# Kernel optimization log

Hardware: AMD Instinct MI355X
Metric: run time of the kernel (lower is better)

Reference implementation:

```python
import jax, jax.numpy as jnp
import numpy as np

B, S, D, H, L = 16, 1024, 128, 8, 3
DFF = 4 * D  # 512
DH = D // H  # 16
NUM_CLASSES = 6


def layernorm(x, g, b, eps):
    mu = jnp.mean(x, axis=-1, keepdims=True)
    var = jnp.mean(jnp.square(x - mu), axis=-1, keepdims=True)
    return g * (x - mu) / jnp.sqrt(var + eps) + b


def setup_inputs() -> dict:
    key = jax.random.key(0)
    ks = jax.random.split(key, 16)
    sc = 0.05
    inp = {
        'x': jax.random.normal(ks[0], (B, S, D), dtype=jnp.float32),
        'Wq': jax.random.normal(ks[1], (L, D, D), dtype=jnp.float32) * sc,
        'bq': jnp.zeros((L, D), dtype=jnp.float32),
        'Wk': jax.random.normal(ks[2], (L, D, D), dtype=jnp.float32) * sc,
        'bk': jnp.zeros((L, D), dtype=jnp.float32),
        'Wv': jax.random.normal(ks[3], (L, D, D), dtype=jnp.float32) * sc,
        'bv': jnp.zeros((L, D), dtype=jnp.float32),
        'ln1_g': jnp.ones((L, D), dtype=jnp.float32),
        'ln1_b': jnp.zeros((L, D), dtype=jnp.float32),
        'W1': jax.random.normal(ks[4], (L, D, DFF), dtype=jnp.float32) * sc,
        'b1': jnp.zeros((L, DFF), dtype=jnp.float32),
        'W2': jax.random.normal(ks[5], (L, DFF, D), dtype=jnp.float32) * sc,
        'b2': jnp.zeros((L, D), dtype=jnp.float32),
        'ln2_g': jnp.ones((L, D), dtype=jnp.float32),
        'ln2_b': jnp.zeros((L, D), dtype=jnp.float32),
        'Wout': jax.random.normal(ks[6], (D, NUM_CLASSES), dtype=jnp.float32) * sc,
        'bout': jnp.zeros((NUM_CLASSES,), dtype=jnp.float32),
    }
    return inp


def reference(x, Wq, bq, Wk, bk, Wv, bv, ln1_g, ln1_b, W1, b1, W2, b2, ln2_g, ln2_b, Wout, bout):
    scale = 1.0 / jnp.sqrt(jnp.float32(DH))
    for l in range(L):
        # Q/K/V projections with ReLU activation (as in source Dense(..., relu))
        q = jax.nn.relu(jnp.einsum('bsd,de->bse', x, Wq[l]) + bq[l])
        k = jax.nn.relu(jnp.einsum('bsd,de->bse', x, Wk[l]) + bk[l])
        v = jax.nn.relu(jnp.einsum('bsd,de->bse', x, Wv[l]) + bv[l])
        # split-heads (tf.split axis=-1 / concat axis=0 == reshape to heads)
        qh = q.reshape(B, S, H, DH)
        kh = k.reshape(B, S, H, DH)
        vh = v.reshape(B, S, H, DH)
        scores = jnp.einsum('bqhd,bkhd->bhqk', qh, kh) * scale  # [B,H,S,S]
        attn = jax.nn.softmax(scores, axis=-1)
        o = jnp.einsum('bhqk,bkhd->bqhd', attn, vh).reshape(B, S, D)
        x = layernorm(o + x, ln1_g[l], ln1_b[l], 1e-8)
        # pointwise FFN (Conv1D kernel_size=1 == dense over last dim)
        h = jax.nn.relu(jnp.einsum('bsd,df->bsf', x, W1[l]) + b1[l])
        f = jnp.einsum('bsf,fd->bsd', h, W2[l]) + b2[l]
        x = layernorm(f + x, ln2_g[l], ln2_b[l], 1e-6)
    return jnp.einsum('bsd,dc->bsc', x, Wout) + bout
```

## Files before the change

kernel.cpp:

```cpp
#include <hip/hip_runtime.h>
#include <math.h>

#define Bq 16
#define Sq 1024
#define Dq 128
#define Hq 8
#define DHq 16
#define DFFq 512
#define Lq 3
#define NCLS 6
#define NROWS (Bq * Sq)
#define NX ((size_t)NROWS * Dq)

typedef __attribute__((ext_vector_type(8))) short    bf16x8;
typedef __attribute__((ext_vector_type(4))) float    f32x4;
typedef __attribute__((ext_vector_type(4))) _Float16 f16x4;
typedef __attribute__((ext_vector_type(8))) _Float16 f16x8;

__device__ inline ushort f32_to_bf16(float f) {
    union { float f; unsigned u; } v; v.f = f;
    unsigned r = v.u + 0x7fffu + ((v.u >> 16) & 1u);
    return (ushort)(r >> 16);
}

__global__ __launch_bounds__(256) void prep_kernel(
    const float* __restrict__ Wqp, const float* __restrict__ Wkp,
    const float* __restrict__ Wvp, const float* __restrict__ W1p,
    const float* __restrict__ W2p, const float* __restrict__ xp,
    ushort* __restrict__ wbf, ushort* __restrict__ xbf)
{
    const int gid = blockIdx.x * 256 + threadIdx.x;
    if (gid < 147456) {
        const int w   = gid / 49152;
        const int rem = gid - w * 49152;
        const int l   = rem >> 14;
        const int idx = rem & 16383;
        const int k   = idx >> 7;
        const int n   = idx & 127;
        const float* src = (w == 0) ? Wqp : (w == 1) ? Wkp : Wvp;
        const float scl = (w == 0) ? 0.25f : 1.0f;
        wbf[(size_t)(w * 3 + l) * 16384 + n * 128 + k] =
            f32_to_bf16(src[(size_t)l * 16384 + k * 128 + n] * scl);
    } else if (gid < 344064) {
        const int g   = gid - 147456;
        const int l   = g >> 16;
        const int idx = g & 65535;
        const int k   = idx >> 9;
        const int n   = idx & 511;
        wbf[147456 + (size_t)l * 65536 + n * 128 + k] =
            f32_to_bf16(W1p[(size_t)l * 65536 + k * 512 + n]);
    } else if (gid < 540672) {
        const int g   = gid - 344064;
        const int l   = g >> 16;
        const int idx = g & 65535;
        const int k   = idx >> 7;
        const int n   = idx & 127;
        wbf[344064 + (size_t)l * 65536 + n * 512 + k] =
            f32_to_bf16(W2p[(size_t)l * 65536 + k * 128 + n]);
    } else {
        const int g = gid - 540672;
        xbf[g] = f32_to_bf16(xp[g]);
    }
}

__global__ __launch_bounds__(256) void gemm_qkv(
    const ushort* __restrict__ A,
    const ushort* __restrict__ wq, const ushort* __restrict__ wk,
    const ushort* __restrict__ wv,
    const float* __restrict__ bqp, const float* __restrict__ bkp,
    const float* __restrict__ bvp,
    _Float16* __restrict__ qo, _Float16* __restrict__ ko,
    _Float16* __restrict__ vo)
{
    __shared__ ushort As[64 * 40];
    __shared__ ushort Bs[128 * 40];

    const int sel  = blockIdx.y;
    const ushort* Bt   = (sel == 0) ? wq : (sel == 1) ? wk : wv;
    const float*  bias = (sel == 0) ? bqp : (sel == 1) ? bkp : bvp;
    const float   bscl = (sel == 0) ? 0.25f : 1.0f;

    const int tid  = threadIdx.x;
    const int row0 = blockIdx.x * 64;
    const int wave = tid >> 6;
    const int lane = tid & 63;
    const int quad = lane >> 4;
    const int m16  = lane & 15;
    const int wm   = wave >> 1;
    const int wn   = wave & 1;

    const int sar = tid >> 2;
    const int sac = (tid & 3) * 8;

    f32x4 acc[2][4];
    #pragma unroll
    for (int i = 0; i < 2; ++i)
        #pragma unroll
        for (int j = 0; j < 4; ++j) acc[i][j] = (f32x4)0.f;

    for (int k0 = 0; k0 < 128; k0 += 32) {
        bf16x8 av = *(const bf16x8*)(A + (size_t)(row0 + sar) * 128 + k0 + sac);
        const int r1 = tid >> 2, r2 = r1 + 64;
        bf16x8 bv1 = *(const bf16x8*)(Bt + (size_t)r1 * 128 + k0 + sac);
        bf16x8 bv2 = *(const bf16x8*)(Bt + (size_t)r2 * 128 + k0 + sac);

        __syncthreads();
        *(bf16x8*)&As[sar * 40 + sac] = av;
        *(bf16x8*)&Bs[r1 * 40 + sac]  = bv1;
        *(bf16x8*)&Bs[r2 * 40 + sac]  = bv2;
        __syncthreads();

        bf16x8 af[2], bf[4];
        #pragma unroll
        for (int i = 0; i < 2; ++i)
            af[i] = *(const bf16x8*)&As[(32 * wm + 16 * i + m16) * 40 + quad * 8];
        #pragma unroll
        for (int j = 0; j < 4; ++j)
            bf[j] = *(const bf16x8*)&Bs[(64 * wn + 16 * j + m16) * 40 + quad * 8];
        #pragma unroll
        for (int i = 0; i < 2; ++i)
            #pragma unroll
            for (int j = 0; j < 4; ++j)
                acc[i][j] = __builtin_amdgcn_mfma_f32_16x16x32_bf16(af[i], bf[j], acc[i][j], 0, 0, 0);
    }

    #pragma unroll
    for (int i = 0; i < 2; ++i) {
        #pragma unroll
        for (int j = 0; j < 4; ++j) {
            const int col = 64 * wn + 16 * j + m16;
            const float bb = bias[col] * bscl;
            const int hh = col >> 4, dh = col & 15;
            #pragma unroll
            for (int r = 0; r < 4; ++r) {
                float val = fmaxf(acc[i][j][r] + bb, 0.f);
                const int gr = row0 + 32 * wm + 16 * i + quad * 4 + r;
                const int b = gr >> 10, s = gr & 1023;
                if (sel == 2) {
                    vo[(((size_t)b * Hq + hh) * DHq + dh) * Sq + s] = (_Float16)val;
                } else {
                    _Float16* outp = (sel == 0) ? qo : ko;
                    outp[(((size_t)b * Hq + hh) * Sq + s) * DHq + dh] = (_Float16)val;
                }
            }
        }
    }
}

__global__ __launch_bounds__(256) void gemm_ffn_fused(
    const float* __restrict__ o, const float* __restrict__ resid,
    const float* __restrict__ g1, const float* __restrict__ beta1,
    const ushort* __restrict__ W1t, const float* __restrict__ bias1,
    const ushort* __restrict__ W2t, const float* __restrict__ bias2,
    const float* __restrict__ g2, const float* __restrict__ beta2,
    float* __restrict__ xb, ushort* __restrict__ xbbf,
    const float* __restrict__ Wout, const float* __restrict__ bout,
    float* __restrict__ out, int last)
{
    __shared__ __align__(16) char smem[69120];
    ushort*    Af   = (ushort*)smem;
    ushort*    Hs   = (ushort*)(smem + 8704);
    ushort*    Bs   = (ushort*)(smem + 41984);
    float*     wo_s = (float*)(smem + 41984);
    _Float16*  vals = (_Float16*)(smem + 60416);
    float*     mus  = (float*)(smem + 68864);
    float*     rsds = (float*)(smem + 68992);

    const int tid  = threadIdx.x;
    const int row0 = blockIdx.x * 32;
    const int wave = tid >> 6;
    const int lane = tid & 63;
    const int quad = lane >> 4;
    const int m16  = lane & 15;
    const int wm   = wave >> 1;
    const int wn   = wave & 1;
    const int sac  = (tid & 3) * 8;
    const int r1   = tid >> 2, r2 = r1 + 64;

    #pragma unroll 2
    for (int it = 0; it < 8; ++it) {
        const int rr = wave * 8 + it;
        const size_t base = (size_t)(row0 + rr) * Dq;
        float v0 = o[base + lane]      + resid[base + lane];
        float v1 = o[base + 64 + lane] + resid[base + 64 + lane];

        float s = v0 + v1;
        #pragma unroll
        for (int off = 32; off > 0; off >>= 1) s += __shfl_xor(s, off, 64);
        const float mu = s * (1.f / 128.f);
        const float d0 = v0 - mu, d1 = v1 - mu;
        float vs = d0 * d0 + d1 * d1;
        #pragma unroll
        for (int off = 32; off > 0; off >>= 1) vs += __shfl_xor(vs, off, 64);
        const float rstd = rsqrtf(vs * (1.f / 128.f) + 1e-8f);

        const float rv0 = g1[lane]      * d0 * rstd + beta1[lane];
        const float rv1 = g1[lane + 64] * d1 * rstd + beta1[lane + 64];
        Af[rr * 136 + lane]       = f32_to_bf16(rv0);
        Af[rr * 136 + 64 + lane]  = f32_to_bf16(rv1);
        vals[rr * 132 + lane]     = (_Float16)rv0;
        vals[rr * 132 + 64 + lane]= (_Float16)rv1;
    }

    f32x4 acc[4];
    #pragma unroll
    for (int j = 0; j < 4; ++j) acc[j] = (f32x4)0.f;

    for (int idx = 0; idx < 8; ++idx) {
        const int cc = idx >> 1;
        const int k0 = (idx & 1) * 64;

        bf16x8 w11 = *(const bf16x8*)(W1t + (size_t)(cc * 128 + r1) * 128 + k0 + sac);
        bf16x8 w12 = *(const bf16x8*)(W1t + (size_t)(cc * 128 + r1) * 128 + k0 + 32 + sac);
        bf16x8 w21 = *(const bf16x8*)(W1t + (size_t)(cc * 128 + r2) * 128 + k0 + sac);
        bf16x8 w22 = *(const bf16x8*)(W1t + (size_t)(cc * 128 + r2) * 128 + k0 + 32 + sac);

        __syncthreads();
        *(bf16x8*)&Bs[r1 * 72 + sac]      = w11;
        *(bf16x8*)&Bs[r1 * 72 + 32 + sac] = w12;
        *(bf16x8*)&Bs[r2 * 72 + sac]      = w21;
        *(bf16x8*)&Bs[r2 * 72 + 32 + sac] = w22;
        __syncthreads();

        #pragma unroll
        for (int h = 0; h < 2; ++h) {
            const int kk = k0 + h * 32;
            const bf16x8 af = *(const bf16x8*)&Af[(16 * wm + m16) * 136 + kk + quad * 8];
            bf16x8 bf[4];
            #pragma unroll
            for (int j = 0; j < 4; ++j)
                bf[j] = *(const bf16x8*)&Bs[(64 * wn + 16 * j + m16) * 72 + h * 32 + quad * 8];
            #pragma unroll
            for (int j = 0; j < 4; ++j)
                acc[j] = __builtin_amdgcn_mfma_f32_16x16x32_bf16(af, bf[j], acc[j], 0, 0, 0);
        }

        if (idx & 1) {
            #pragma unroll
            for (int j = 0; j < 4; ++j) {
                const int col = cc * 128 + 64 * wn + 16 * j + m16;
                const float bb = bias1[col];
                #pragma unroll
                for (int r = 0; r < 4; ++r) {
                    const int row = 16 * wm + quad * 4 + r;
                    Hs[row * 520 + col] = f32_to_bf16(fmaxf(acc[j][r] + bb, 0.f));
                }
                acc[j] = (f32x4)0.f;
            }
        }
    }

    f32x4 acc2[4];
    #pragma unroll
    for (int j = 0; j < 4; ++j) acc2[j] = (f32x4)0.f;

    for (int kc = 0; kc < 8; ++kc) {
        const int k0 = kc * 64;

        bf16x8 w11 = *(const bf16x8*)(W2t + (size_t)r1 * DFFq + k0 + sac);
        bf16x8 w12 = *(const bf16x8*)(W2t + (size_t)r1 * DFFq + k0 + 32 + sac);
        bf16x8 w21 = *(const bf16x8*)(W2t + (size_t)r2 * DFFq + k0 + sac);
        bf16x8 w22 = *(const bf16x8*)(W2t + (size_t)r2 * DFFq + k0 + 32 + sac);

        __syncthreads();
        *(bf16x8*)&Bs[r1 * 72 + sac]      = w11;
        *(bf16x8*)&Bs[r1 * 72 + 32 + sac] = w12;
        *(bf16x8*)&Bs[r2 * 72 + sac]      = w21;
        *(bf16x8*)&Bs[r2 * 72 + 32 + sac] = w22;
        __syncthreads();

        #pragma unroll
        for (int h = 0; h < 2; ++h) {
            const int kk = k0 + h * 32;
            const bf16x8 af = *(const bf16x8*)&Hs[(16 * wm + m16) * 520 + kk + quad * 8];
            bf16x8 bf[4];
            #pragma unroll
            for (int j = 0; j < 4; ++j)
                bf[j] = *(const bf16x8*)&Bs[(64 * wn + 16 * j + m16) * 72 + h * 32 + quad * 8];
            #pragma unroll
            for (int j = 0; j < 4; ++j)
                acc2[j] = __builtin_amdgcn_mfma_f32_16x16x32_bf16(af, bf[j], acc2[j], 0, 0, 0);
        }
    }

    __syncthreads();

    float vreg[4][4];
    #pragma unroll
    for (int j = 0; j < 4; ++j) {
        const int col = 64 * wn + 16 * j + m16;
        const float bb = bias2[col];
        #pragma unroll
        for (int r = 0; r < 4; ++r) {
            const int row = 16 * wm + quad * 4 + r;
            float v = acc2[j][r] + bb + (float)vals[row * 132 + col];
            vreg[j][r] = v;
            vals[row * 132 + col] = (_Float16)v;
        }
    }
    if (last) {
        #pragma unroll
        for (int i = 0; i < 3; ++i) wo_s[tid + i * 256] = Wout[tid + i * 256];
    }
    __syncthreads();

    if (tid < 32) {
        float s = 0.f, s2 = 0.f;
        #pragma unroll 8
        for (int c = 0; c < Dq; ++c) {
            float x = (float)vals[tid * 132 + c];
            s += x; s2 = fmaf(x, x, s2);
        }
        const float mu  = s * (1.f / 128.f);
        const float var = s2 * (1.f / 128.f) - mu * mu;
        mus[tid]  = mu;
        rsds[tid] = rsqrtf(var + 1e-6f);
    }
    __syncthreads();

    if (!last) {
        #pragma unroll
        for (int j = 0; j < 4; ++j) {
            const int col = 64 * wn + 16 * j + m16;
            #pragma unroll
            for (int r = 0; r < 4; ++r) {
                const int row = 16 * wm + quad * 4 + r;
                const float rn = g2[col] * (vreg[j][r] - mus[row]) * rsds[row] + beta2[col];
                const size_t idx = (size_t)(row0 + row) * Dq + col;
                xb[idx]   = rn;
                xbbf[idx] = f32_to_bf16(rn);
            }
        }
    } else {
        #pragma unroll
        for (int j = 0; j < 4; ++j) {
            const int col = 64 * wn + 16 * j + m16;
            #pragma unroll
            for (int r = 0; r < 4; ++r) {
                const int row = 16 * wm + quad * 4 + r;
                vals[row * 132 + col] =
                    (_Float16)(g2[col] * (vreg[j][r] - mus[row]) * rsds[row] + beta2[col]);
            }
        }
        __syncthreads();
        if (tid < 32 * NCLS) {
            const int row = tid / NCLS;
            const int c   = tid - row * NCLS;
            float a = bout[c];
            #pragma unroll 8
            for (int kk = 0; kk < Dq; ++kk)
                a = fmaf((float)vals[row * 132 + kk], wo_s[kk * NCLS + c], a);
            out[(size_t)(row0 + row) * NCLS + c] = a;
        }
    }
}

__global__ __launch_bounds__(256) void attn_mfma(
    const _Float16* __restrict__ q, const _Float16* __restrict__ k,
    const _Float16* __restrict__ vt, float* __restrict__ o)
{
    __shared__ _Float16 Ks[256 * 20];
    __shared__ _Float16 Vs[16 * 264];

    const int bh   = blockIdx.x;
    const int qc   = blockIdx.y;
    const int b    = bh >> 3;
    const int h    = bh & 7;
    const int tid  = threadIdx.x;
    const int wave = tid >> 6;
    const int lane = tid & 63;
    const int quad = lane >> 4;
    const int m16  = lane & 15;
    const int q0   = qc * 128 + wave * 32;

    const f16x4 qf0 = *(const f16x4*)(q + (((size_t)bh * Sq) + q0 + m16) * DHq + quad * 4);
    const f16x4 qf1 = *(const f16x4*)(q + (((size_t)bh * Sq) + q0 + 16 + m16) * DHq + quad * 4);

    const _Float16* kg  = k  + (size_t)bh * Sq * DHq;
    const _Float16* vtg = vt + (size_t)bh * DHq * Sq;

    f32x4 oacc0 = (f32x4)0.f, oacc1 = (f32x4)0.f;
    float lacc0 = 0.f, lacc1 = 0.f;

    const int krow = tid;
    const int vrow = tid >> 4;
    const int vcol = (tid & 15) * 16;

    for (int kb = 0; kb < 4; ++kb) {
        f16x8 ka  = *(const f16x8*)(kg + ((size_t)kb * 256 + krow) * DHq);
        f16x8 kb8 = *(const f16x8*)(kg + ((size_t)kb * 256 + krow) * DHq + 8);
        f16x8 va  = *(const f16x8*)(vtg + (size_t)vrow * Sq + kb * 256 + vcol);
        f16x8 vb  = *(const f16x8*)(vtg + (size_t)vrow * Sq + kb * 256 + vcol + 8);
        __syncthreads();
        *(f16x8*)&Ks[krow * 20 + 0] = ka;
        *(f16x8*)&Ks[krow * 20 + 8] = kb8;
        *(f16x8*)&Vs[vrow * 264 + vcol + 0] = va;
        *(f16x8*)&Vs[vrow * 264 + vcol + 8] = vb;
        __syncthreads();

        #pragma unroll 4
        for (int kt = 0; kt < 16; ++kt) {
            const f16x4 kf = *(const f16x4*)&Ks[(kt * 16 + m16) * 20 + quad * 4];
            const f16x4 vf = *(const f16x4*)&Vs[m16 * 264 + kt * 16 + quad * 4];

            f32x4 st0 = __builtin_amdgcn_mfma_f32_16x16x16f16(kf, qf0, (f32x4)0.f, 0, 0, 0);
            f32x4 st1 = __builtin_amdgcn_mfma_f32_16x16x16f16(kf, qf1, (f32x4)0.f, 0, 0, 0);

            float p00 = __expf(st0[0]);
            float p01 = __expf(st0[1]);
            float p02 = __expf(st0[2]);
            float p03 = __expf(st0[3]);
            float p10 = __expf(st1[0]);
            float p11 = __expf(st1[1]);
            float p12 = __expf(st1[2]);
            float p13 = __expf(st1[3]);
            lacc0 += (p00 + p01) + (p02 + p03);
            lacc1 += (p10 + p11) + (p12 + p13);

            f16x4 pf0, pf1;
            pf0[0] = (_Float16)p00; pf0[1] = (_Float16)p01;
            pf0[2] = (_Float16)p02; pf0[3] = (_Float16)p03;
            pf1[0] = (_Float16)p10; pf1[1] = (_Float16)p11;
            pf1[2] = (_Float16)p12; pf1[3] = (_Float16)p13;

            oacc0 = __builtin_amdgcn_mfma_f32_16x16x16f16(pf0, vf, oacc0, 0, 0, 0);
            oacc1 = __builtin_amdgcn_mfma_f32_16x16x16f16(pf1, vf, oacc1, 0, 0, 0);
        }
    }

    lacc0 += __shfl_xor(lacc0, 16, 64);
    lacc0 += __shfl_xor(lacc0, 32, 64);
    lacc1 += __shfl_xor(lacc1, 16, 64);
    lacc1 += __shfl_xor(lacc1, 32, 64);

    #pragma unroll
    for (int r = 0; r < 4; ++r) {
        const float ls0 = __shfl(lacc0, quad * 4 + r, 64);
        const float ls1 = __shfl(lacc1, quad * 4 + r, 64);
        o[((size_t)b * Sq + q0 + quad * 4 + r) * Dq + h * DHq + m16]      = oacc0[r] / ls0;
        o[((size_t)b * Sq + q0 + 16 + quad * 4 + r) * Dq + h * DHq + m16] = oacc1[r] / ls1;
    }
}

extern "C" void kernel_launch(void* const* d_in, const int* in_sizes, int n_in,
                              void* d_out, int out_size, void* d_ws, size_t ws_size,
                              hipStream_t stream)
{
    const float* x_in  = (const float*)d_in[0];
    const float* Wq    = (const float*)d_in[1];
    const float* bq    = (const float*)d_in[2];
    const float* Wk    = (const float*)d_in[3];
    const float* bk    = (const float*)d_in[4];
    const float* Wv    = (const float*)d_in[5];
    const float* bv    = (const float*)d_in[6];
    const float* ln1_g = (const float*)d_in[7];
    const float* ln1_b = (const float*)d_in[8];
    const float* W1    = (const float*)d_in[9];
    const float* b1    = (const float*)d_in[10];
    const float* W2    = (const float*)d_in[11];
    const float* b2    = (const float*)d_in[12];
    const float* ln2_g = (const float*)d_in[13];
    const float* ln2_b = (const float*)d_in[14];
    const float* Wout  = (const float*)d_in[15];
    const float* bout  = (const float*)d_in[16];
    float* out = (float*)d_out;

    float* ws = (float*)d_ws;
    _Float16* qf16 = (_Float16*)ws;
    _Float16* kf16 = (_Float16*)(ws + NX / 2);
    _Float16* vt16 = (_Float16*)(ws + NX);
    float*    xb   = ws + 9 * NX / 2;
    ushort*   xbf0 = (ushort*)(ws + 11 * NX / 2);
    ushort*   xbbf = (ushort*)(ws + 13 * NX / 2);
    ushort*   wbf  = (ushort*)(ws + 7 * NX);
    float*    obuf = ws + 8 * NX;

    prep_kernel<<<dim3(10304), dim3(256), 0, stream>>>(Wq, Wk, Wv, W1, W2, x_in, wbf, xbf0);

    const dim3 blk(256);
    const float* xcur = x_in;
    const ushort* xcur_bf = xbf0;

    for (int l = 0; l < Lq; ++l) {
        const ushort* wqt = wbf + (size_t)(0 * 3 + l) * 16384;
        const ushort* wkt = wbf + (size_t)(1 * 3 + l) * 16384;
        const ushort* wvt = wbf + (size_t)(2 * 3 + l) * 16384;
        const ushort* w1t = wbf + 147456 + (size_t)l * 65536;
        const ushort* w2t = wbf + 344064 + (size_t)l * 65536;

        gemm_qkv<<<dim3(256, 3), blk, 0, stream>>>(
            xcur_bf, wqt, wkt, wvt, bq + l * Dq, bk + l * Dq, bv + l * Dq,
            qf16, kf16, vt16);

        attn_mfma<<<dim3(Bq * Hq, 8), blk, 0, stream>>>(qf16, kf16, vt16, obuf);

        gemm_ffn_fused<<<dim3(512), blk, 0, stream>>>(
            obuf, xcur, ln1_g + l * Dq, ln1_b + l * Dq,
            w1t, b1 + l * DFFq, w2t, b2 + l * Dq,
            ln2_g + l * Dq, ln2_b + l * Dq,
            xb, xbbf, Wout, bout, out, (l == Lq - 1) ? 1 : 0);

        xcur = xb;
        xcur_bf = xbbf;
    }
}
```

Measured before the change: 275.9 us.

## Fuse all layers into one persistent cooperative kernel with grid syncs

Replaces the ten separate launches (prep, then qkv/attention/ffn per layer) with a single cooperative persistent kernel of 512 blocks that loops over the work units of each stage and uses grid-wide barriers between stages. This targets per-launch overhead and the gaps between kernels. In exchange, every block is sized for the largest shared-memory stage, stages with uneven unit counts (768 qkv tiles, 1024 attention units) leave some blocks idle, and grid syncs have their own cost. If the cooperative launch fails, the code falls back to the old multi-kernel path.

```diff
diff --git a/kernel.cpp b/kernel.cpp
--- a/kernel.cpp
+++ b/kernel.cpp
@@ -1,5 +1,8 @@
 #include <hip/hip_runtime.h>
+#include <hip/hip_cooperative_groups.h>
 #include <math.h>
+
+namespace cg = cooperative_groups;
 
 #define Bq 16
 #define Sq 1024
@@ -11,6 +14,7 @@
 #define NCLS 6
 #define NROWS (Bq * Sq)
 #define NX ((size_t)NROWS * Dq)
+#define PREP_N 2637824
 
 typedef __attribute__((ext_vector_type(8))) short    bf16x8;
 typedef __attribute__((ext_vector_type(4))) float    f32x4;
@@ -23,13 +27,13 @@
     return (ushort)(r >> 16);
 }
 
-__global__ __launch_bounds__(256) void prep_kernel(
+__device__ __forceinline__ void prep_one(
+    int gid,
     const float* __restrict__ Wqp, const float* __restrict__ Wkp,
     const float* __restrict__ Wvp, const float* __restrict__ W1p,
     const float* __restrict__ W2p, const float* __restrict__ xp,
     ushort* __restrict__ wbf, ushort* __restrict__ xbf)
 {
-    const int gid = blockIdx.x * 256 + threadIdx.x;
     if (gid < 147456) {
         const int w   = gid / 49152;
         const int rem = gid - w * 49152;
@@ -63,7 +67,8 @@
     }
 }
 
-__global__ __launch_bounds__(256) void gemm_qkv(
+__device__ __forceinline__ void qkv_tile(
+    char* smem, int sel, int row0,
     const ushort* __restrict__ A,
     const ushort* __restrict__ wq, const ushort* __restrict__ wk,
     const ushort* __restrict__ wv,
@@ -72,25 +77,23 @@
     _Float16* __restrict__ qo, _Float16* __restrict__ ko,
     _Float16* __restrict__ vo)
 {
-    __shared__ ushort As[64 * 40];
-    __shared__ ushort Bs[128 * 40];
-
-    const int sel  = blockIdx.y;
+    ushort* As = (ushort*)smem;
+    ushort* Bs = (ushort*)smem + 2560;
+
     const ushort* Bt   = (sel == 0) ? wq : (sel == 1) ? wk : wv;
     const float*  bias = (sel == 0) ? bqp : (sel == 1) ? bkp : bvp;
     const float   bscl = (sel == 0) ? 0.25f : 1.0f;
 
     const int tid  = threadIdx.x;
-    const int row0 = blockIdx.x * 64;
     const int wave = tid >> 6;
     const int lane = tid & 63;
     const int quad = lane >> 4;
     const int m16  = lane & 15;
     const int wm   = wave >> 1;
     const int wn   = wave & 1;
-
-    const int sar = tid >> 2;
-    const int sac = (tid & 3) * 8;
+    const int sar  = tid >> 2;
+    const int sac  = (tid & 3) * 8;
+    const int r1   = tid >> 2, r2 = r1 + 64;
 
     f32x4 acc[2][4];
     #pragma unroll
@@ -99,8 +102,7 @@
         for (int j = 0; j < 4; ++j) acc[i][j] = (f32x4)0.f;
 
     for (int k0 = 0; k0 < 128; k0 += 32) {
-        bf16x8 av = *(const bf16x8*)(A + (size_t)(row0 + sar) * 128 + k0 + sac);
-        const int r1 = tid >> 2, r2 = r1 + 64;
+        bf16x8 av  = *(const bf16x8*)(A + (size_t)(row0 + sar) * 128 + k0 + sac);
         bf16x8 bv1 = *(const bf16x8*)(Bt + (size_t)r1 * 128 + k0 + sac);
         bf16x8 bv2 = *(const bf16x8*)(Bt + (size_t)r2 * 128 + k0 + sac);
 
@@ -147,7 +149,94 @@
     }
 }
 
-__global__ __launch_bounds__(256) void gemm_ffn_fused(
+__device__ __forceinline__ void attn_unit(
+    char* smem, int bh, int qc,
+    const _Float16* __restrict__ q, const _Float16* __restrict__ k,
+    const _Float16* __restrict__ vt, float* __restrict__ o)
+{
+    _Float16* Ks = (_Float16*)smem;
+    _Float16* Vs = (_Float16*)(smem + 10240);
+
+    const int b    = bh >> 3;
+    const int h    = bh & 7;
+    const int tid  = threadIdx.x;
+    const int wave = tid >> 6;
+    const int lane = tid & 63;
+    const int quad = lane >> 4;
+    const int m16  = lane & 15;
+    const int q0   = qc * 128 + wave * 32;
+
+    const f16x4 qf0 = *(const f16x4*)(q + (((size_t)bh * Sq) + q0 + m16) * DHq + quad * 4);
+    const f16x4 qf1 = *(const f16x4*)(q + (((size_t)bh * Sq) + q0 + 16 + m16) * DHq + quad * 4);
+
+    const _Float16* kg  = k  + (size_t)bh * Sq * DHq;
+    const _Float16* vtg = vt + (size_t)bh * DHq * Sq;
+
+    f32x4 oacc0 = (f32x4)0.f, oacc1 = (f32x4)0.f;
+    float lacc0 = 0.f, lacc1 = 0.f;
+
+    const int krow = tid;
+    const int vrow = tid >> 4;
+    const int vcol = (tid & 15) * 16;
+
+    for (int kb = 0; kb < 4; ++kb) {
+        f16x8 ka  = *(const f16x8*)(kg + ((size_t)kb * 256 + krow) * DHq);
+        f16x8 kb8 = *(const f16x8*)(kg + ((size_t)kb * 256 + krow) * DHq + 8);
+        f16x8 va  = *(const f16x8*)(vtg + (size_t)vrow * Sq + kb * 256 + vcol);
+        f16x8 vb  = *(const f16x8*)(vtg + (size_t)vrow * Sq + kb * 256 + vcol + 8);
+        __syncthreads();
+        *(f16x8*)&Ks[krow * 20 + 0] = ka;
+        *(f16x8*)&Ks[krow * 20 + 8] = kb8;
+        *(f16x8*)&Vs[vrow * 264 + vcol + 0] = va;
+        *(f16x8*)&Vs[vrow * 264 + vcol + 8] = vb;
+        __syncthreads();
+
+        #pragma unroll 4
+        for (int kt = 0; kt < 16; ++kt) {
+            const f16x4 kf = *(const f16x4*)&Ks[(kt * 16 + m16) * 20 + quad * 4];
+            const f16x4 vf = *(const f16x4*)&Vs[m16 * 264 + kt * 16 + quad * 4];
+
+            f32x4 st0 = __builtin_amdgcn_mfma_f32_16x16x16f16(kf, qf0, (f32x4)0.f, 0, 0, 0);
+            f32x4 st1 = __builtin_amdgcn_mfma_f32_16x16x16f16(kf, qf1, (f32x4)0.f, 0, 0, 0);
+
+            float p00 = __expf(st0[0]);
+            float p01 = __expf(st0[1]);
+            float p02 = __expf(st0[2]);
+            float p03 = __expf(st0[3]);
+            float p10 = __expf(st1[0]);
+            float p11 = __expf(st1[1]);
+            float p12 = __expf(st1[2]);
+            float p13 = __expf(st1[3]);
+            lacc0 += (p00 + p01) + (p02 + p03);
+            lacc1 += (p10 + p11) + (p12 + p13);
+
+            f16x4 pf0, pf1;
+            pf0[0] = (_Float16)p00; pf0[1] = (_Float16)p01;
+            pf0[2] = (_Float16)p02; pf0[3] = (_Float16)p03;
+            pf1[0] = (_Float16)p10; pf1[1] = (_Float16)p11;
+            pf1[2] = (_Float16)p12; pf1[3] = (_Float16)p13;
+
+            oacc0 = __builtin_amdgcn_mfma_f32_16x16x16f16(pf0, vf, oacc0, 0, 0, 0);
+            oacc1 = __builtin_amdgcn_mfma_f32_16x16x16f16(pf1, vf, oacc1, 0, 0, 0);
+        }
+    }
+
+    lacc0 += __shfl_xor(lacc0, 16, 64);
+    lacc0 += __shfl_xor(lacc0, 32, 64);
+    lacc1 += __shfl_xor(lacc1, 16, 64);
+    lacc1 += __shfl_xor(lacc1, 32, 64);
+
+    #pragma unroll
+    for (int r = 0; r < 4; ++r) {
+        const float ls0 = __shfl(lacc0, quad * 4 + r, 64);
+        const float ls1 = __shfl(lacc1, quad * 4 + r, 64);
+        o[((size_t)b * Sq + q0 + quad * 4 + r) * Dq + h * DHq + m16]      = oacc0[r] / ls0;
+        o[((size_t)b * Sq + q0 + 16 + quad * 4 + r) * Dq + h * DHq + m16] = oacc1[r] / ls1;
+    }
+}
+
+__device__ __forceinline__ void ffn_unit(
+    char* smem, int row0,
     const float* __restrict__ o, const float* __restrict__ resid,
     const float* __restrict__ g1, const float* __restrict__ beta1,
     const ushort* __restrict__ W1t, const float* __restrict__ bias1,
@@ -157,7 +246,6 @@
     const float* __restrict__ Wout, const float* __restrict__ bout,
     float* __restrict__ out, int last)
 {
-    __shared__ __align__(16) char smem[69120];
     ushort*    Af   = (ushort*)smem;
     ushort*    Hs   = (ushort*)(smem + 8704);
     ushort*    Bs   = (ushort*)(smem + 41984);
@@ -167,7 +255,6 @@
     float*     rsds = (float*)(smem + 68992);
 
     const int tid  = threadIdx.x;
-    const int row0 = blockIdx.x * 32;
     const int wave = tid >> 6;
     const int lane = tid & 63;
     const int quad = lane >> 4;
@@ -196,10 +283,10 @@
 
         const float rv0 = g1[lane]      * d0 * rstd + beta1[lane];
         const float rv1 = g1[lane + 64] * d1 * rstd + beta1[lane + 64];
-        Af[rr * 136 + lane]       = f32_to_bf16(rv0);
-        Af[rr * 136 + 64 + lane]  = f32_to_bf16(rv1);
-        vals[rr * 132 + lane]     = (_Float16)rv0;
-        vals[rr * 132 + 64 + lane]= (_Float16)rv1;
+        Af[rr * 136 + lane]        = f32_to_bf16(rv0);
+        Af[rr * 136 + 64 + lane]   = f32_to_bf16(rv1);
+        vals[rr * 132 + lane]      = (_Float16)rv0;
+        vals[rr * 132 + 64 + lane] = (_Float16)rv1;
     }
 
     f32x4 acc[4];
@@ -223,13 +310,13 @@
         __syncthreads();
 
         #pragma unroll
-        for (int h = 0; h < 2; ++h) {
-            const int kk = k0 + h * 32;
+        for (int hh = 0; hh < 2; ++hh) {
+            const int kk = k0 + hh * 32;
             const bf16x8 af = *(const bf16x8*)&Af[(16 * wm + m16) * 136 + kk + quad * 8];
             bf16x8 bf[4];
             #pragma unroll
             for (int j = 0; j < 4; ++j)
-                bf[j] = *(const bf16x8*)&Bs[(64 * wn + 16 * j + m16) * 72 + h * 32 + quad * 8];
+                bf[j] = *(const bf16x8*)&Bs[(64 * wn + 16 * j + m16) * 72 + hh * 32 + quad * 8];
             #pragma unroll
             for (int j = 0; j < 4; ++j)
                 acc[j] = __builtin_amdgcn_mfma_f32_16x16x32_bf16(af, bf[j], acc[j], 0, 0, 0);
@@ -270,13 +357,13 @@
         __syncthreads();
 
         #pragma unroll
-        for (int h = 0; h < 2; ++h) {
-            const int kk = k0 + h * 32;
+        for (int hh = 0; hh < 2; ++hh) {
+            const int kk = k0 + hh * 32;
             const bf16x8 af = *(const bf16x8*)&Hs[(16 * wm + m16) * 520 + kk + quad * 8];
             bf16x8 bf[4];
             #pragma unroll
             for (int j = 0; j < 4; ++j)
-                bf[j] = *(const bf16x8*)&Bs[(64 * wn + 16 * j + m16) * 72 + h * 32 + quad * 8];
+                bf[j] = *(const bf16x8*)&Bs[(64 * wn + 16 * j + m16) * 72 + hh * 32 + quad * 8];
             #pragma unroll
             for (int j = 0; j < 4; ++j)
                 acc2[j] = __builtin_amdgcn_mfma_f32_16x16x32_bf16(af, bf[j], acc2[j], 0, 0, 0);
@@ -355,91 +442,91 @@
     }
 }
 
-__global__ __launch_bounds__(256) void attn_mfma(
-    const _Float16* __restrict__ q, const _Float16* __restrict__ k,
-    const _Float16* __restrict__ vt, float* __restrict__ o)
-{
-    __shared__ _Float16 Ks[256 * 20];
-    __shared__ _Float16 Vs[16 * 264];
-
-    const int bh   = blockIdx.x;
-    const int qc   = blockIdx.y;
-    const int b    = bh >> 3;
-    const int h    = bh & 7;
-    const int tid  = threadIdx.x;
-    const int wave = tid >> 6;
-    const int lane = tid & 63;
-    const int quad = lane >> 4;
-    const int m16  = lane & 15;
-    const int q0   = qc * 128 + wave * 32;
-
-    const f16x4 qf0 = *(const f16x4*)(q + (((size_t)bh * Sq) + q0 + m16) * DHq + quad * 4);
-    const f16x4 qf1 = *(const f16x4*)(q + (((size_t)bh * Sq) + q0 + 16 + m16) * DHq + quad * 4);
-
-    const _Float16* kg  = k  + (size_t)bh * Sq * DHq;
-    const _Float16* vtg = vt + (size_t)bh * DHq * Sq;
-
-    f32x4 oacc0 = (f32x4)0.f, oacc1 = (f32x4)0.f;
-    float lacc0 = 0.f, lacc1 = 0.f;
-
-    const int krow = tid;
-    const int vrow = tid >> 4;
-    const int vcol = (tid & 15) * 16;
-
-    for (int kb = 0; kb < 4; ++kb) {
-        f16x8 ka  = *(const f16x8*)(kg + ((size_t)kb * 256 + krow) * DHq);
-        f16x8 kb8 = *(const f16x8*)(kg + ((size_t)kb * 256 + krow) * DHq + 8);
-        f16x8 va  = *(const f16x8*)(vtg + (size_t)vrow * Sq + kb * 256 + vcol);
-        f16x8 vb  = *(const f16x8*)(vtg + (size_t)vrow * Sq + kb * 256 + vcol + 8);
-        __syncthreads();
-        *(f16x8*)&Ks[krow * 20 + 0] = ka;
-        *(f16x8*)&Ks[krow * 20 + 8] = kb8;
-        *(f16x8*)&Vs[vrow * 264 + vcol + 0] = va;
-        *(f16x8*)&Vs[vrow * 264 + vcol + 8] = vb;
-        __syncthreads();
-
-        #pragma unroll 4
-        for (int kt = 0; kt < 16; ++kt) {
-            const f16x4 kf = *(const f16x4*)&Ks[(kt * 16 + m16) * 20 + quad * 4];
-            const f16x4 vf = *(const f16x4*)&Vs[m16 * 264 + kt * 16 + quad * 4];
-
-            f32x4 st0 = __builtin_amdgcn_mfma_f32_16x16x16f16(kf, qf0, (f32x4)0.f, 0, 0, 0);
-            f32x4 st1 = __builtin_amdgcn_mfma_f32_16x16x16f16(kf, qf1, (f32x4)0.f, 0, 0, 0);
-
-            float p00 = __expf(st0[0]);
-            float p01 = __expf(st0[1]);
-            float p02 = __expf(st0[2]);
-            float p03 = __expf(st0[3]);
-            float p10 = __expf(st1[0]);
-            float p11 = __expf(st1[1]);
-            float p12 = __expf(st1[2]);
-            float p13 = __expf(st1[3]);
-            lacc0 += (p00 + p01) + (p02 + p03);
-            lacc1 += (p10 + p11) + (p12 + p13);
-
-            f16x4 pf0, pf1;
-            pf0[0] = (_Float16)p00; pf0[1] = (_Float16)p01;
-            pf0[2] = (_Float16)p02; pf0[3] = (_Float16)p03;
-            pf1[0] = (_Float16)p10; pf1[1] = (_Float16)p11;
-            pf1[2] = (_Float16)p12; pf1[3] = (_Float16)p13;
-
-            oacc0 = __builtin_amdgcn_mfma_f32_16x16x16f16(pf0, vf, oacc0, 0, 0, 0);
-            oacc1 = __builtin_amdgcn_mfma_f32_16x16x16f16(pf1, vf, oacc1, 0, 0, 0);
-        }
-    }
-
-    lacc0 += __shfl_xor(lacc0, 16, 64);
-    lacc0 += __shfl_xor(lacc0, 32, 64);
-    lacc1 += __shfl_xor(lacc1, 16, 64);
-    lacc1 += __shfl_xor(lacc1, 32, 64);
-
-    #pragma unroll
-    for (int r = 0; r < 4; ++r) {
-        const float ls0 = __shfl(lacc0, quad * 4 + r, 64);
-        const float ls1 = __shfl(lacc1, quad * 4 + r, 64);
-        o[((size_t)b * Sq + q0 + quad * 4 + r) * Dq + h * DHq + m16]      = oacc0[r] / ls0;
-        o[((size_t)b * Sq + q0 + 16 + quad * 4 + r) * Dq + h * DHq + m16] = oacc1[r] / ls1;
-    }
+struct MegaArgs {
+    const float *x_in, *Wq, *bq, *Wk, *bk, *Wv, *bv;
+    const float *ln1_g, *ln1_b, *W1, *b1, *W2, *b2, *ln2_g, *ln2_b, *Wout, *bout;
+    float* out;
+    ushort* wbf; ushort* xbf0;
+    _Float16 *qf16, *kf16, *vt16;
+    float* obuf; float* xb; ushort* xbbf;
+};
+
+__global__ __launch_bounds__(256, 2) void mega_kernel(MegaArgs a)
+{
+    __shared__ __align__(16) char smem[69120];
+    cg::grid_group grid = cg::this_grid();
+    const int tid = threadIdx.x;
+
+    for (int gid = blockIdx.x * 256 + tid; gid < PREP_N; gid += 512 * 256)
+        prep_one(gid, a.Wq, a.Wk, a.Wv, a.W1, a.W2, a.x_in, a.wbf, a.xbf0);
+    grid.sync();
+
+    for (int l = 0; l < Lq; ++l) {
+        const ushort* wqt = a.wbf + (size_t)(0 * 3 + l) * 16384;
+        const ushort* wkt = a.wbf + (size_t)(1 * 3 + l) * 16384;
+        const ushort* wvt = a.wbf + (size_t)(2 * 3 + l) * 16384;
+        const ushort* w1t = a.wbf + 147456 + (size_t)l * 65536;
+        const ushort* w2t = a.wbf + 344064 + (size_t)l * 65536;
+        const ushort* xcur_bf = (l == 0) ? a.xbf0 : a.xbbf;
+        const float*  resid   = (l == 0) ? a.x_in : a.xb;
+
+        for (int u = blockIdx.x; u < 768; u += 512)
+            qkv_tile(smem, u >> 8, (u & 255) * 64, xcur_bf, wqt, wkt, wvt,
+                     a.bq + l * Dq, a.bk + l * Dq, a.bv + l * Dq,
+                     a.qf16, a.kf16, a.vt16);
+        grid.sync();
+
+        for (int u = blockIdx.x; u < 1024; u += 512)
+            attn_unit(smem, u >> 3, u & 7, a.qf16, a.kf16, a.vt16, a.obuf);
+        grid.sync();
+
+        ffn_unit(smem, blockIdx.x * 32, a.obuf, resid,
+                 a.ln1_g + l * Dq, a.ln1_b + l * Dq,
+                 w1t, a.b1 + l * DFFq, w2t, a.b2 + l * Dq,
+                 a.ln2_g + l * Dq, a.ln2_b + l * Dq,
+                 a.xb, a.xbbf, a.Wout, a.bout, a.out, (l == Lq - 1) ? 1 : 0);
+        if (l < Lq - 1) grid.sync();
+    }
+}
+
+__global__ __launch_bounds__(256) void prep_kernel_fb(
+    const float* Wqp, const float* Wkp, const float* Wvp,
+    const float* W1p, const float* W2p, const float* xp,
+    ushort* wbf, ushort* xbf)
+{
+    const int gid = blockIdx.x * 256 + threadIdx.x;
+    if (gid < PREP_N)
+        prep_one(gid, Wqp, Wkp, Wvp, W1p, W2p, xp, wbf, xbf);
+}
+
+__global__ __launch_bounds__(256) void qkv_kernel_fb(
+    const ushort* A, const ushort* wq, const ushort* wk, const ushort* wv,
+    const float* bqp, const float* bkp, const float* bvp,
+    _Float16* qo, _Float16* ko, _Float16* vo)
+{
+    __shared__ __align__(16) char smem[15360];
+    qkv_tile(smem, blockIdx.y, blockIdx.x * 64, A, wq, wk, wv, bqp, bkp, bvp, qo, ko, vo);
+}
+
+__global__ __launch_bounds__(256) void attn_kernel_fb(
+    const _Float16* q, const _Float16* k, const _Float16* vt, float* o)
+{
+    __shared__ __align__(16) char smem[18688];
+    attn_unit(smem, blockIdx.x, blockIdx.y, q, k, vt, o);
+}
+
+__global__ __launch_bounds__(256) void ffn_kernel_fb(
+    const float* o, const float* resid,
+    const float* g1, const float* beta1,
+    const ushort* W1t, const float* bias1,
+    const ushort* W2t, const float* bias2,
+    const float* g2, const float* beta2,
+    float* xb, ushort* xbbf,
+    const float* Wout, const float* bout, float* out, int last)
+{
+    __shared__ __align__(16) char smem[69120];
+    ffn_unit(smem, blockIdx.x * 32, o, resid, g1, beta1, W1t, bias1,
+             W2t, bias2, g2, beta2, xb, xbbf, Wout, bout, out, last);
 }
 
 extern "C" void kernel_launch(void* const* d_in, const int* in_sizes, int n_in,
@@ -475,32 +562,43 @@
     ushort*   wbf  = (ushort*)(ws + 7 * NX);
     float*    obuf = ws + 8 * NX;
 
-    prep_kernel<<<dim3(10304), dim3(256), 0, stream>>>(Wq, Wk, Wv, W1, W2, x_in, wbf, xbf0);
-
-    const dim3 blk(256);
-    const float* xcur = x_in;
-    const ushort* xcur_bf = xbf0;
-
-    for (int l = 0; l < Lq; ++l) {
-        const ushort* wqt = wbf + (size_t)(0 * 3 + l) * 16384;
-        const ushort* wkt = wbf + (size_t)(1 * 3 + l) * 16384;
-        const ushort* wvt = wbf + (size_t)(2 * 3 + l) * 16384;
-        const ushort* w1t = wbf + 147456 + (size_t)l * 65536;
-        const ushort* w2t = wbf + 344064 + (size_t)l * 65536;
-
-        gemm_qkv<<<dim3(256, 3), blk, 0, stream>>>(
-            xcur_bf, wqt, wkt, wvt, bq + l * Dq, bk + l * Dq, bv + l * Dq,
-            qf16, kf16, vt16);
-
-        attn_mfma<<<dim3(Bq * Hq, 8), blk, 0, stream>>>(qf16, kf16, vt16, obuf);
-
-        gemm_ffn_fused<<<dim3(512), blk, 0, stream>>>(
-            obuf, xcur, ln1_g + l * Dq, ln1_b + l * Dq,
-            w1t, b1 + l * DFFq, w2t, b2 + l * Dq,
-            ln2_g + l * Dq, ln2_b + l * Dq,
-            xb, xbbf, Wout, bout, out, (l == Lq - 1) ? 1 : 0);
-
-        xcur = xb;
-        xcur_bf = xbbf;
-    }
-}
+    MegaArgs margs;
+    margs.x_in = x_in; margs.Wq = Wq; margs.bq = bq; margs.Wk = Wk; margs.bk = bk;
+    margs.Wv = Wv; margs.bv = bv; margs.ln1_g = ln1_g; margs.ln1_b = ln1_b;
+    margs.W1 = W1; margs.b1 = b1; margs.W2 = W2; margs.b2 = b2;
+    margs.ln2_g = ln2_g; margs.ln2_b = ln2_b; margs.Wout = Wout; margs.bout = bout;
+    margs.out = out; margs.wbf = wbf; margs.xbf0 = xbf0;
+    margs.qf16 = qf16; margs.kf16 = kf16; margs.vt16 = vt16;
+    margs.obuf = obuf; margs.xb = xb; margs.xbbf = xbbf;
+
+    void* kargs[] = { &margs };
+    hipError_t err = hipLaunchCooperativeKernel((const void*)mega_kernel,
+                                                dim3(512), dim3(256), kargs, 0, stream);
+    if (err != hipSuccess) {
+        (void)hipGetLastError();
+        const dim3 blk(256);
+        prep_kernel_fb<<<dim3(10304), blk, 0, stream>>>(Wq, Wk, Wv, W1, W2, x_in, wbf, xbf0);
+        const float* xcur = x_in;
+        const ushort* xcur_bf = xbf0;
+        for (int l = 0; l < Lq; ++l) {
+            const ushort* wqt = wbf + (size_t)(0 * 3 + l) * 16384;
+            const ushort* wkt = wbf + (size_t)(1 * 3 + l) * 16384;
+            const ushort* wvt = wbf + (size_t)(2 * 3 + l) * 16384;
+            const ushort* w1t = wbf + 147456 + (size_t)l * 65536;
+            const ushort* w2t = wbf + 344064 + (size_t)l * 65536;
+
+            qkv_kernel_fb<<<dim3(256, 3), blk, 0, stream>>>(
+                xcur_bf, wqt, wkt, wvt, bq + l * Dq, bk + l * Dq, bv + l * Dq,
+                qf16, kf16, vt16);
+            attn_kernel_fb<<<dim3(Bq * Hq, 8), blk, 0, stream>>>(qf16, kf16, vt16, obuf);
+            ffn_kernel_fb<<<dim3(512), blk, 0, stream>>>(
+                obuf, xcur, ln1_g + l * Dq, ln1_b + l * Dq,
+                w1t, b1 + l * DFFq, w2t, b2 + l * Dq,
+                ln2_g + l * Dq, ln2_b + l * Dq,
+                xb, xbbf, Wout, bout, out, (l == Lq - 1) ? 1 : 0);
+
+            xcur = xb;
+            xcur_bf = xbbf;
+        }
+    }
+}
```

New measurement: 814.9 us. 195% more time.

## Fuse next layer's QKV projection into FFN kernel epilogue

Applied to the files above, without the earlier changes.

The FFN kernel now keeps the layer-norm output as bf16 in shared memory and computes the next layer's Q, K and V projections in place. It writes them directly in the head-split fp16 layouts that the attention kernel expects. Only the first layer still launches the standalone QKV GEMM. This removes two kernel launches and the global write and reread of the bf16 activation copy. In exchange, the FFN kernel grows longer and adds more synchronisation, and the QKV work now runs over 512 blocks instead of the 768 the standalone kernel used.

```diff
diff --git a/kernel.cpp b/kernel.cpp
--- a/kernel.cpp
+++ b/kernel.cpp
@@ -153,7 +153,13 @@
     const ushort* __restrict__ W1t, const float* __restrict__ bias1,
     const ushort* __restrict__ W2t, const float* __restrict__ bias2,
     const float* __restrict__ g2, const float* __restrict__ beta2,
-    float* __restrict__ xb, ushort* __restrict__ xbbf,
+    float* __restrict__ xb,
+    const ushort* __restrict__ wqn, const ushort* __restrict__ wkn,
+    const ushort* __restrict__ wvn,
+    const float* __restrict__ bqn, const float* __restrict__ bkn,
+    const float* __restrict__ bvn,
+    _Float16* __restrict__ qo, _Float16* __restrict__ ko,
+    _Float16* __restrict__ vo, int do_next,
     const float* __restrict__ Wout, const float* __restrict__ bout,
     float* __restrict__ out, int last)
 {
@@ -196,10 +202,10 @@
 
         const float rv0 = g1[lane]      * d0 * rstd + beta1[lane];
         const float rv1 = g1[lane + 64] * d1 * rstd + beta1[lane + 64];
-        Af[rr * 136 + lane]       = f32_to_bf16(rv0);
-        Af[rr * 136 + 64 + lane]  = f32_to_bf16(rv1);
-        vals[rr * 132 + lane]     = (_Float16)rv0;
-        vals[rr * 132 + 64 + lane]= (_Float16)rv1;
+        Af[rr * 136 + lane]        = f32_to_bf16(rv0);
+        Af[rr * 136 + 64 + lane]   = f32_to_bf16(rv1);
+        vals[rr * 132 + lane]      = (_Float16)rv0;
+        vals[rr * 132 + 64 + lane] = (_Float16)rv1;
     }
 
     f32x4 acc[4];
@@ -223,13 +229,13 @@
         __syncthreads();
 
         #pragma unroll
-        for (int h = 0; h < 2; ++h) {
-            const int kk = k0 + h * 32;
+        for (int hh = 0; hh < 2; ++hh) {
+            const int kk = k0 + hh * 32;
             const bf16x8 af = *(const bf16x8*)&Af[(16 * wm + m16) * 136 + kk + quad * 8];
             bf16x8 bf[4];
             #pragma unroll
             for (int j = 0; j < 4; ++j)
-                bf[j] = *(const bf16x8*)&Bs[(64 * wn + 16 * j + m16) * 72 + h * 32 + quad * 8];
+                bf[j] = *(const bf16x8*)&Bs[(64 * wn + 16 * j + m16) * 72 + hh * 32 + quad * 8];
             #pragma unroll
             for (int j = 0; j < 4; ++j)
                 acc[j] = __builtin_amdgcn_mfma_f32_16x16x32_bf16(af, bf[j], acc[j], 0, 0, 0);
@@ -270,13 +276,13 @@
         __syncthreads();
 
         #pragma unroll
-        for (int h = 0; h < 2; ++h) {
-            const int kk = k0 + h * 32;
+        for (int hh = 0; hh < 2; ++hh) {
+            const int kk = k0 + hh * 32;
             const bf16x8 af = *(const bf16x8*)&Hs[(16 * wm + m16) * 520 + kk + quad * 8];
             bf16x8 bf[4];
             #pragma unroll
             for (int j = 0; j < 4; ++j)
-                bf[j] = *(const bf16x8*)&Bs[(64 * wn + 16 * j + m16) * 72 + h * 32 + quad * 8];
+                bf[j] = *(const bf16x8*)&Bs[(64 * wn + 16 * j + m16) * 72 + hh * 32 + quad * 8];
             #pragma unroll
             for (int j = 0; j < 4; ++j)
                 acc2[j] = __builtin_amdgcn_mfma_f32_16x16x32_bf16(af, bf[j], acc2[j], 0, 0, 0);
@@ -326,9 +332,67 @@
             for (int r = 0; r < 4; ++r) {
                 const int row = 16 * wm + quad * 4 + r;
                 const float rn = g2[col] * (vreg[j][r] - mus[row]) * rsds[row] + beta2[col];
-                const size_t idx = (size_t)(row0 + row) * Dq + col;
-                xb[idx]   = rn;
-                xbbf[idx] = f32_to_bf16(rn);
+                xb[(size_t)(row0 + row) * Dq + col] = rn;
+                Af[row * 136 + col] = f32_to_bf16(rn);
+            }
+        }
+
+        if (do_next) {
+            for (int sel = 0; sel < 3; ++sel) {
+                const ushort* Bt   = (sel == 0) ? wqn : (sel == 1) ? wkn : wvn;
+                const float*  bias = (sel == 0) ? bqn : (sel == 1) ? bkn : bvn;
+                const float   bscl = (sel == 0) ? 0.25f : 1.0f;
+
+                f32x4 qacc[4];
+                #pragma unroll
+                for (int j = 0; j < 4; ++j) qacc[j] = (f32x4)0.f;
+
+                for (int half = 0; half < 2; ++half) {
+                    const int k0 = half * 64;
+                    bf16x8 w11 = *(const bf16x8*)(Bt + (size_t)r1 * 128 + k0 + sac);
+                    bf16x8 w12 = *(const bf16x8*)(Bt + (size_t)r1 * 128 + k0 + 32 + sac);
+                    bf16x8 w21 = *(const bf16x8*)(Bt + (size_t)r2 * 128 + k0 + sac);
+                    bf16x8 w22 = *(const bf16x8*)(Bt + (size_t)r2 * 128 + k0 + 32 + sac);
+
+                    __syncthreads();
+                    *(bf16x8*)&Bs[r1 * 72 + sac]      = w11;
+                    *(bf16x8*)&Bs[r1 * 72 + 32 + sac] = w12;
+                    *(bf16x8*)&Bs[r2 * 72 + sac]      = w21;
+                    *(bf16x8*)&Bs[r2 * 72 + 32 + sac] = w22;
+                    __syncthreads();
+
+                    #pragma unroll
+                    for (int hh = 0; hh < 2; ++hh) {
+                        const int kk = k0 + hh * 32;
+                        const bf16x8 af = *(const bf16x8*)&Af[(16 * wm + m16) * 136 + kk + quad * 8];
+                        bf16x8 bf[4];
+                        #pragma unroll
+                        for (int j = 0; j < 4; ++j)
+                            bf[j] = *(const bf16x8*)&Bs[(64 * wn + 16 * j + m16) * 72 + hh * 32 + quad * 8];
+                        #pragma unroll
+                        for (int j = 0; j < 4; ++j)
+                            qacc[j] = __builtin_amdgcn_mfma_f32_16x16x32_bf16(af, bf[j], qacc[j], 0, 0, 0);
+                    }
+                }
+
+                #pragma unroll
+                for (int j = 0; j < 4; ++j) {
+                    const int col = 64 * wn + 16 * j + m16;
+                    const float bb = bias[col] * bscl;
+                    const int hh = col >> 4, dh = col & 15;
+                    #pragma unroll
+                    for (int r = 0; r < 4; ++r) {
+                        float val = fmaxf(qacc[j][r] + bb, 0.f);
+                        const int gr = row0 + 16 * wm + quad * 4 + r;
+                        const int b = gr >> 10, s = gr & 1023;
+                        if (sel == 2) {
+                            vo[(((size_t)b * Hq + hh) * DHq + dh) * Sq + s] = (_Float16)val;
+                        } else {
+                            _Float16* outp = (sel == 0) ? qo : ko;
+                            outp[(((size_t)b * Hq + hh) * Sq + s) * DHq + dh] = (_Float16)val;
+                        }
+                    }
+                }
             }
         }
     } else {
@@ -471,26 +535,33 @@
     _Float16* vt16 = (_Float16*)(ws + NX);
     float*    xb   = ws + 9 * NX / 2;
     ushort*   xbf0 = (ushort*)(ws + 11 * NX / 2);
-    ushort*   xbbf = (ushort*)(ws + 13 * NX / 2);
     ushort*   wbf  = (ushort*)(ws + 7 * NX);
     float*    obuf = ws + 8 * NX;
 
     prep_kernel<<<dim3(10304), dim3(256), 0, stream>>>(Wq, Wk, Wv, W1, W2, x_in, wbf, xbf0);
 
     const dim3 blk(256);
+
+    {
+        const ushort* wqt = wbf + (size_t)0 * 16384;
+        const ushort* wkt = wbf + (size_t)3 * 16384;
+        const ushort* wvt = wbf + (size_t)6 * 16384;
+        gemm_qkv<<<dim3(256, 3), blk, 0, stream>>>(
+            xbf0, wqt, wkt, wvt, bq, bk, bv, qf16, kf16, vt16);
+    }
+
     const float* xcur = x_in;
-    const ushort* xcur_bf = xbf0;
-
     for (int l = 0; l < Lq; ++l) {
-        const ushort* wqt = wbf + (size_t)(0 * 3 + l) * 16384;
-        const ushort* wkt = wbf + (size_t)(1 * 3 + l) * 16384;
-        const ushort* wvt = wbf + (size_t)(2 * 3 + l) * 16384;
         const ushort* w1t = wbf + 147456 + (size_t)l * 65536;
         const ushort* w2t = wbf + 344064 + (size_t)l * 65536;
-
-        gemm_qkv<<<dim3(256, 3), blk, 0, stream>>>(
-            xcur_bf, wqt, wkt, wvt, bq + l * Dq, bk + l * Dq, bv + l * Dq,
-            qf16, kf16, vt16);
+        const int next = (l < Lq - 1) ? 1 : 0;
+        const int ln   = l + 1;
+        const ushort* wqn = next ? (wbf + (size_t)(0 * 3 + ln) * 16384) : wbf;
+        const ushort* wkn = next ? (wbf + (size_t)(1 * 3 + ln) * 16384) : wbf;
+        const ushort* wvn = next ? (wbf + (size_t)(2 * 3 + ln) * 16384) : wbf;
+        const float*  bqn = next ? (bq + ln * Dq) : bq;
+        const float*  bkn = next ? (bk + ln * Dq) : bk;
+        const float*  bvn = next ? (bv + ln * Dq) : bv;
 
         attn_mfma<<<dim3(Bq * Hq, 8), blk, 0, stream>>>(qf16, kf16, vt16, obuf);
 
@@ -498,9 +569,11 @@
             obuf, xcur, ln1_g + l * Dq, ln1_b + l * Dq,
             w1t, b1 + l * DFFq, w2t, b2 + l * Dq,
             ln2_g + l * Dq, ln2_b + l * Dq,
-            xb, xbbf, Wout, bout, out, (l == Lq - 1) ? 1 : 0);
+            xb,
+            wqn, wkn, wvn, bqn, bkn, bvn,
+            qf16, kf16, vt16, next,
+            Wout, bout, out, (l == Lq - 1) ? 1 : 0);
 
         xcur = xb;
-        xcur_bf = xbbf;
     }
 }
```

Result: faster. 264.5 us (-4.1%).
